# Optimization experiments

Measured on AMD Instinct MI355X. Metric: run time of the kernel, lower is better.

Reference implementation:

```python
import jax, jax.numpy as jnp
import numpy as np

N, E, D, H, DH, M = 100000, 1600000, 128, 8, 16, 3  # nodes, edges, model_dim, heads, head_dim, views
NEG = -1e9


def setup_inputs() -> dict:
    key = jax.random.key(0)
    ks = jax.random.split(key, 12)
    x = jax.random.normal(ks[0], (N, D), jnp.float32)
    src = jax.random.randint(ks[1], (E,), 0, N)
    dst = jax.random.randint(ks[2], (E,), 0, N)
    pi = jax.random.uniform(ks[3], (N, H, M), jnp.float32)
    pi = pi / pi.sum(-1, keepdims=True)  # router mixture over views
    view_w = jax.random.uniform(ks[4], (E, M), jnp.float32)
    s = 1.0 / np.sqrt(D)
    Wq = jax.random.normal(ks[5], (D, D), jnp.float32) * s
    Wk = jax.random.normal(ks[6], (D, D), jnp.float32) * s
    Wv = jax.random.normal(ks[7], (D, D), jnp.float32) * s
    bq = jax.random.normal(ks[8], (D,), jnp.float32) * 0.02
    bk = jax.random.normal(ks[9], (D,), jnp.float32) * 0.02
    bv = jax.random.normal(ks[10], (D,), jnp.float32) * 0.02
    return {"x": x, "pi": pi, "view_w": view_w, "Wq": Wq, "bq": bq,
            "Wk": Wk, "bk": bk, "Wv": Wv, "bv": bv, "src": src, "dst": dst}


def reference(x, pi, view_w, Wq, bq, Wk, bk, Wv, bv, src, dst):
    n = x.shape[0]
    q = (x @ Wq + bq).reshape(n, H, DH)
    k = (x @ Wk + bk).reshape(n, H, DH)
    v = (x @ Wv + bv).reshape(n, H, DH)
    # per-edge mixture weight: sum over views of pi[dst] * view_w  -> [E, H]
    mix = jnp.einsum('ehm,em->eh', pi[dst], view_w)
    raw = jnp.einsum('ehd,ehd->eh', q[dst], k[src]) / jnp.sqrt(jnp.float32(DH))
    scores = raw + jnp.log(jnp.clip(mix, 1e-8))  # adjacency_mode == 'bias'
    valid = mix > 0
    masked = jnp.where(valid, scores, NEG)
    # scatter-softmax over incoming edges per (node, head)
    smax = jax.ops.segment_max(masked, dst, num_segments=n)
    expv = jnp.where(valid, jnp.exp(masked - smax[dst]), 0.0)
    ssum = jax.ops.segment_sum(expv, dst, num_segments=n)
    attn = expv / jnp.maximum(ssum[dst], 1e-8)  # [E, H]
    # weighted scatter-sum aggregation -> [N, H, DH]
    node_states = jax.ops.segment_sum(v[src] * attn[:, :, None], dst, num_segments=n)
    return node_states, attn
```

## Files before the change

### kernel.cpp

```cpp
#include <hip/hip_runtime.h>
#include <hip/hip_bf16.h>
#include <math.h>

#define SCAN_CHUNK 2048

typedef _Float16 half8 __attribute__((ext_vector_type(8)));
typedef _Float16 half16v __attribute__((ext_vector_type(16)));
typedef float floatx4 __attribute__((ext_vector_type(4)));


__global__ void hist_kernel(const int* __restrict__ dst, int* __restrict__ counts, int e) {
    int i = blockIdx.x * blockDim.x + threadIdx.x;
    if (i < e) atomicAdd(&counts[dst[i]], 1);
}

__global__ __launch_bounds__(256) void scan_block_sums(const int* __restrict__ counts,
                                                       int* __restrict__ bsum, int n) {
    __shared__ int sd[256];
    int t = threadIdx.x;
    int base = blockIdx.x * SCAN_CHUNK + t * 8;
    int s = 0;
#pragma unroll
    for (int j = 0; j < 8; ++j) {
        int idx = base + j;
        if (idx < n) s += counts[idx];
    }
    sd[t] = s;
    __syncthreads();
    for (int off = 128; off > 0; off >>= 1) {
        if (t < off) sd[t] += sd[t + off];
        __syncthreads();
    }
    if (t == 0) bsum[blockIdx.x] = sd[0];
}

__global__ void scan_wave(int* bsum, int nb) {
    int lane = threadIdx.x;
    int orig = (lane < nb) ? bsum[lane] : 0;
    int v = orig;
    for (int off = 1; off < 64; off <<= 1) {
        int t = __shfl_up(v, off, 64);
        if (lane >= off) v += t;
    }
    if (lane < nb) bsum[lane] = v - orig;
}

__global__ __launch_bounds__(256) void scan_write(const int* __restrict__ counts,
                                                  const int* __restrict__ bsum,
                                                  int* __restrict__ row_ptr,
                                                  int* __restrict__ cursor,
                                                  int n, int total) {
    __shared__ int sd[256];
    int t = threadIdx.x;
    int base = blockIdx.x * SCAN_CHUNK + t * 8;
    int v[8];
    int s = 0;
#pragma unroll
    for (int j = 0; j < 8; ++j) {
        int idx = base + j;
        v[j] = (idx < n) ? counts[idx] : 0;
        s += v[j];
    }
    sd[t] = s;
    __syncthreads();
    for (int off = 1; off < 256; off <<= 1) {
        int tmp = 0;
        if (t >= off) tmp = sd[t - off];
        __syncthreads();
        if (t >= off) sd[t] += tmp;
        __syncthreads();
    }
    int run = bsum[blockIdx.x] + sd[t] - s;
#pragma unroll
    for (int j = 0; j < 8; ++j) {
        int idx = base + j;
        if (idx < n) {
            row_ptr[idx] = run;
            cursor[idx] = run;
            run += v[j];
        }
    }
    if (blockIdx.x == 0 && t == 0) row_ptr[n] = total;
}

__global__ void fill_csr(const int* __restrict__ dst, int* cursor,
                         int* __restrict__ csr, int e) {
    int i = blockIdx.x * blockDim.x + threadIdx.x;
    if (i < e) {
        int p = atomicAdd(&cursor[dst[i]], 1);
        csr[p] = i;
    }
}


__global__ __launch_bounds__(256) void convert_x(const float* __restrict__ x,
                                                 _Float16* __restrict__ xh, int total8) {
    int i = blockIdx.x * blockDim.x + threadIdx.x;
    if (i < total8) {
        const float4* s = (const float4*)x + i * 2;
        float4 a = s[0], b = s[1];
        half8 h;
        h[0] = (_Float16)a.x; h[1] = (_Float16)a.y; h[2] = (_Float16)a.z; h[3] = (_Float16)a.w;
        h[4] = (_Float16)b.x; h[5] = (_Float16)b.y; h[6] = (_Float16)b.z; h[7] = (_Float16)b.w;
        *((half8*)xh + i) = h;
    }
}

__global__ __launch_bounds__(256) void prep_w(const float* __restrict__ Wq,
                                              const float* __restrict__ Wk,
                                              const float* __restrict__ Wv,
                                              _Float16* __restrict__ wt) {
    const float* W = (blockIdx.x == 0) ? Wq : (blockIdx.x == 1) ? Wk : Wv;
    _Float16* out = wt + (size_t)blockIdx.x * 16384;
    int t = threadIdx.x;
    for (int r = 0; r < 64; ++r) {
        int idx = r * 256 + t;
        int k = idx >> 7, nn = idx & 127;
        out[nn * 128 + k] = (_Float16)W[idx];
    }
}


#define LDP 136

__global__ __launch_bounds__(256) void qkv_mfma(
    const _Float16* __restrict__ xh, const _Float16* __restrict__ wt,
    const float* __restrict__ bq, const float* __restrict__ bk,
    const float* __restrict__ bv,
    _Float16* __restrict__ qh, _Float16* __restrict__ kh, _Float16* __restrict__ vh,
    int n) {
    __shared__ __align__(16) _Float16 xs[128 * LDP];
    __shared__ __align__(16) _Float16 ws[128 * LDP];

    int t = threadIdx.x;
    int tile0 = blockIdx.x * 128;
    int sel = blockIdx.y;
    const _Float16* wsel = wt + (size_t)sel * 16384;
    const float* bias = (sel == 0) ? bq : (sel == 1) ? bk : bv;
    _Float16* out = (sel == 0) ? qh : (sel == 1) ? kh : vh;

#pragma unroll
    for (int r = 0; r < 8; ++r) {
        int id = r * 256 + t;
        int row = id >> 4, c8 = id & 15;
        int grow = tile0 + row;
        half8 val = (half8)(_Float16)0;
        if (grow < n) val = *((const half8*)(xh + (size_t)grow * 128) + c8);
        *((half8*)(xs + row * LDP) + c8) = val;
        half8 wv = *((const half8*)(wsel + row * 128) + c8);
        *((half8*)(ws + row * LDP) + c8) = wv;
    }
    __syncthreads();

    int wave = t >> 6, lane = t & 63;
    int wm = (wave & 1) * 64, wn = (wave >> 1) * 64;
    int lrow = lane & 15, quad = lane >> 4;

    floatx4 acc[4][4];
#pragma unroll
    for (int i = 0; i < 4; ++i)
#pragma unroll
        for (int j = 0; j < 4; ++j) acc[i][j] = (floatx4)0.f;

#pragma unroll
    for (int kk = 0; kk < 4; ++kk) {
        int kbase = kk * 32 + quad * 8;
        half8 a[4], b[4];
#pragma unroll
        for (int i = 0; i < 4; ++i)
            a[i] = *(const half8*)(xs + (wm + i * 16 + lrow) * LDP + kbase);
#pragma unroll
        for (int j = 0; j < 4; ++j)
            b[j] = *(const half8*)(ws + (wn + j * 16 + lrow) * LDP + kbase);
#pragma unroll
        for (int i = 0; i < 4; ++i)
#pragma unroll
            for (int j = 0; j < 4; ++j)
                acc[i][j] = __builtin_amdgcn_mfma_f32_16x16x32_f16(a[i], b[j], acc[i][j], 0, 0, 0);
    }

#pragma unroll
    for (int i = 0; i < 4; ++i) {
#pragma unroll
        for (int j = 0; j < 4; ++j) {
            int col = wn + j * 16 + lrow;
            float bv_ = bias[col];
#pragma unroll
            for (int r = 0; r < 4; ++r) {
                int row = wm + i * 16 + quad * 4 + r;
                int grow = tile0 + row;
                if (grow < n) out[(size_t)grow * 128 + col] = (_Float16)(acc[i][j][r] + bv_);
            }
        }
    }
}


__global__ __launch_bounds__(256) void edge_attn(
    const _Float16* __restrict__ qh, const _Float16* __restrict__ kh,
    const _Float16* __restrict__ vh, const float* __restrict__ pi,
    const float* __restrict__ view_w, const int* __restrict__ src,
    const int* __restrict__ row_ptr, const int* __restrict__ csr,
    float* __restrict__ node_out, float* __restrict__ invb,
    _Float16* __restrict__ pbuf, int n) {
    int t = threadIdx.x;
    int node = blockIdx.x * 32 + (t >> 3);
    int h = t & 7;
    if (node >= n) return;

    half16v qv = *(const half16v*)(qh + (size_t)node * 128 + h * 16);
    float qf[16];
#pragma unroll
    for (int j = 0; j < 16; ++j) qf[j] = (float)qv[j];

    float p0 = pi[node * 24 + h * 3 + 0];
    float p1 = pi[node * 24 + h * 3 + 1];
    float p2 = pi[node * 24 + h * 3 + 2];
    int beg = row_ptr[node], end = row_ptr[node + 1];

    float l = 0.f;
    float acc[16];
#pragma unroll
    for (int j = 0; j < 16; ++j) acc[j] = 0.f;

    int e_n = 0, s_n = 0;
    float wa_n = 0.f, wb_n = 0.f, wc_n = 0.f;
    if (beg < end) {
        e_n = csr[beg]; s_n = src[e_n];
        const float* vp_ = view_w + (size_t)e_n * 3;
        wa_n = vp_[0]; wb_n = vp_[1]; wc_n = vp_[2];
    }

    for (int i = beg; i < end; ++i) {
        int e = e_n, s0 = s_n;
        float wa = wa_n, wb = wb_n, wc = wc_n;

        const half16v* kp = (const half16v*)(kh + (size_t)s0 * 128 + h * 16);
        half16v kv = kp[0];
        const half16v* vp = (const half16v*)(vh + (size_t)s0 * 128 + h * 16);
        half16v vv = vp[0];

        if (i + 1 < end) {
            e_n = csr[i + 1]; s_n = src[e_n];
            const float* vpn = view_w + (size_t)e_n * 3;
            wa_n = vpn[0]; wb_n = vpn[1]; wc_n = vpn[2];
        }

        float mix = fmaf(p0, wa, fmaf(p1, wb, p2 * wc));
        float d = 0.f;
#pragma unroll
        for (int j = 0; j < 16; ++j) d = fmaf(qf[j], (float)kv[j], d);

        float p = (mix > 0.f) ? mix * __expf(d * 0.25f) : 0.f;
        pbuf[(size_t)e * 8 + h] = (_Float16)p;
        l += p;
#pragma unroll
        for (int j = 0; j < 16; ++j) acc[j] = fmaf(p, (float)vv[j], acc[j]);
    }

    float inv = 1.f / fmaxf(l, 1e-8f);
    invb[(size_t)node * 8 + h] = inv;

    float4* op = (float4*)(node_out + (size_t)node * 128 + h * 16);
#pragma unroll
    for (int j = 0; j < 4; ++j)
        op[j] = make_float4(acc[4 * j] * inv, acc[4 * j + 1] * inv,
                            acc[4 * j + 2] * inv, acc[4 * j + 3] * inv);
}


__global__ __launch_bounds__(256) void attn_norm(
    const _Float16* __restrict__ pbuf, const int* __restrict__ dst,
    const float* __restrict__ invb, float* __restrict__ attn_out, int e) {
    int i = blockIdx.x * blockDim.x + threadIdx.x;
    if (i < e) {
        int d = dst[i];
        half8 p = *((const half8*)pbuf + i);
        const float4* iv = (const float4*)(invb + (size_t)d * 8);
        float4 i0 = iv[0], i1 = iv[1];
        float4* op = (float4*)(attn_out + (size_t)i * 8);
        op[0] = make_float4((float)p[0] * i0.x, (float)p[1] * i0.y,
                            (float)p[2] * i0.z, (float)p[3] * i0.w);
        op[1] = make_float4((float)p[4] * i1.x, (float)p[5] * i1.y,
                            (float)p[6] * i1.z, (float)p[7] * i1.w);
    }
}


extern "C" void kernel_launch(void* const* d_in, const int* in_sizes, int n_in,
                              void* d_out, int out_size, void* d_ws, size_t ws_size,
                              hipStream_t stream) {
    const float* x  = (const float*)d_in[0];
    const float* pi = (const float*)d_in[1];
    const float* vw = (const float*)d_in[2];
    const float* Wq = (const float*)d_in[3];
    const float* bq = (const float*)d_in[4];
    const float* Wk = (const float*)d_in[5];
    const float* bk = (const float*)d_in[6];
    const float* Wv = (const float*)d_in[7];
    const float* bv = (const float*)d_in[8];
    const int* src  = (const int*)d_in[9];
    const int* dst  = (const int*)d_in[10];

    int n = in_sizes[0] / 128;
    int e = in_sizes[9];

    _Float16* xh = (_Float16*)d_ws;
    _Float16* qh = xh + (size_t)n * 128;
    _Float16* kh = qh + (size_t)n * 128;
    _Float16* vh = kh + (size_t)n * 128;
    _Float16* wt = vh + (size_t)n * 128;
    _Float16* pbuf = wt + 3 * 16384;
    float* invb  = (float*)(pbuf + (size_t)e * 8);
    int* counts  = (int*)(invb + (size_t)n * 8);
    int* cursor  = counts + n;
    int* row_ptr = cursor + n;
    int* csr     = row_ptr + n + 1;
    int* bsum    = csr + e;

    float* node_out = (float*)d_out;
    float* attn_out = node_out + (size_t)n * 128;

    hipMemsetAsync(counts, 0, (size_t)n * sizeof(int), stream);

    int eb = (e + 255) / 256;
    hist_kernel<<<eb, 256, 0, stream>>>(dst, counts, e);

    int nb = (n + SCAN_CHUNK - 1) / SCAN_CHUNK;
    scan_block_sums<<<nb, 256, 0, stream>>>(counts, bsum, n);
    scan_wave<<<1, 64, 0, stream>>>(bsum, nb);
    scan_write<<<nb, 256, 0, stream>>>(counts, bsum, row_ptr, cursor, n, e);
    fill_csr<<<eb, 256, 0, stream>>>(dst, cursor, csr, e);

    int tot8 = (n * 128) / 8;
    convert_x<<<(tot8 + 255) / 256, 256, 0, stream>>>(x, xh, tot8);
    prep_w<<<3, 256, 0, stream>>>(Wq, Wk, Wv, wt);

    int gtiles = (n + 127) / 128;
    qkv_mfma<<<dim3(gtiles, 3), 256, 0, stream>>>(xh, wt, bq, bk, bv, qh, kh, vh, n);

    int gb = (n + 31) / 32;
    edge_attn<<<gb, 256, 0, stream>>>(qh, kh, vh, pi, vw, src, row_ptr, csr,
                                      node_out, invb, pbuf, n);
    attn_norm<<<eb, 256, 0, stream>>>(pbuf, dst, invb, attn_out, e);
}
```

Measured before the change: 669.7 us.

## Sort nodes by in-degree for balanced edge attention and deepen K/V prefetch

Adds a degree histogram, a scan and a scatter that build a permutation of nodes ordered by in-degree. edge_attn then processes nodes in descending-degree order, so nodes in the same wavefront have similar loop trip counts and less divergence. The edge loop also prefetches K/V rows one edge ahead and indices two edges ahead, and uses the fdot2 builtin for the q·k dot product. The cost is three extra small kernels plus a memset, and a node order that scatters writes to node_out and invb rather than keeping them contiguous.

```diff
diff --git a/kernel.cpp b/kernel.cpp
--- a/kernel.cpp
+++ b/kernel.cpp
@@ -3,10 +3,18 @@
 #include <math.h>
 
 #define SCAN_CHUNK 2048
-
+#define DEG_BINS 256
+
+typedef _Float16 half2v __attribute__((ext_vector_type(2)));
 typedef _Float16 half8 __attribute__((ext_vector_type(8)));
 typedef _Float16 half16v __attribute__((ext_vector_type(16)));
 typedef float floatx4 __attribute__((ext_vector_type(4)));
+
+#if defined(__has_builtin)
+#if __has_builtin(__builtin_amdgcn_fdot2)
+#define USE_FDOT2 1
+#endif
+#endif
 
 
 __global__ void hist_kernel(const int* __restrict__ dst, int* __restrict__ counts, int e) {
@@ -89,6 +97,46 @@
     if (i < e) {
         int p = atomicAdd(&cursor[dst[i]], 1);
         csr[p] = i;
+    }
+}
+
+
+__global__ __launch_bounds__(256) void deg_hist(const int* __restrict__ counts,
+                                                int* __restrict__ bins, int n) {
+    int i = blockIdx.x * blockDim.x + threadIdx.x;
+    if (i < n) {
+        int d = counts[i];
+        if (d > DEG_BINS - 1) d = DEG_BINS - 1;
+        atomicAdd(&bins[d], 1);
+    }
+}
+
+__global__ __launch_bounds__(256) void deg_scan(const int* __restrict__ bins,
+                                                int* __restrict__ bcur) {
+    __shared__ int sd[256];
+    int t = threadIdx.x;
+    int v = bins[t];
+    sd[t] = v;
+    __syncthreads();
+    for (int off = 1; off < 256; off <<= 1) {
+        int tmp = 0;
+        if (t >= off) tmp = sd[t - off];
+        __syncthreads();
+        if (t >= off) sd[t] += tmp;
+        __syncthreads();
+    }
+    bcur[t] = sd[t] - v;
+}
+
+__global__ __launch_bounds__(256) void deg_scatter(const int* __restrict__ counts,
+                                                   int* __restrict__ bcur,
+                                                   int* __restrict__ perm, int n) {
+    int i = blockIdx.x * blockDim.x + threadIdx.x;
+    if (i < n) {
+        int d = counts[i];
+        if (d > DEG_BINS - 1) d = DEG_BINS - 1;
+        int p = atomicAdd(&bcur[d], 1);
+        perm[p] = i;
     }
 }
 
@@ -201,17 +249,18 @@
     const _Float16* __restrict__ vh, const float* __restrict__ pi,
     const float* __restrict__ view_w, const int* __restrict__ src,
     const int* __restrict__ row_ptr, const int* __restrict__ csr,
+    const int* __restrict__ perm,
     float* __restrict__ node_out, float* __restrict__ invb,
     _Float16* __restrict__ pbuf, int n) {
     int t = threadIdx.x;
-    int node = blockIdx.x * 32 + (t >> 3);
+    int gid = blockIdx.x * 32 + (t >> 3);
+    if (gid >= n) return;
+    int node = perm[n - 1 - gid];
     int h = t & 7;
-    if (node >= n) return;
-
-    half16v qv = *(const half16v*)(qh + (size_t)node * 128 + h * 16);
-    float qf[16];
-#pragma unroll
-    for (int j = 0; j < 16; ++j) qf[j] = (float)qv[j];
+
+    const half16v qv = *(const half16v*)(qh + (size_t)node * 128 + h * 16);
+    const _Float16* kbase = kh + h * 16;
+    const _Float16* vbase = vh + h * 16;
 
     float p0 = pi[node * 24 + h * 3 + 0];
     float p1 = pi[node * 24 + h * 3 + 1];
@@ -223,39 +272,62 @@
 #pragma unroll
     for (int j = 0; j < 16; ++j) acc[j] = 0.f;
 
-    int e_n = 0, s_n = 0;
-    float wa_n = 0.f, wb_n = 0.f, wc_n = 0.f;
+    int e0 = 0, s0 = 0, e1 = 0, s1 = 0;
+    float w0a = 0.f, w0b = 0.f, w0c = 0.f;
+    float w1a = 0.f, w1b = 0.f, w1c = 0.f;
+    half16v kc = (half16v)(_Float16)0, vc = (half16v)(_Float16)0;
+
     if (beg < end) {
-        e_n = csr[beg]; s_n = src[e_n];
-        const float* vp_ = view_w + (size_t)e_n * 3;
-        wa_n = vp_[0]; wb_n = vp_[1]; wc_n = vp_[2];
+        e0 = csr[beg]; s0 = src[e0];
+        const float* vp = view_w + (size_t)e0 * 3;
+        w0a = vp[0]; w0b = vp[1]; w0c = vp[2];
+        kc = *(const half16v*)(kbase + (size_t)s0 * 128);
+        vc = *(const half16v*)(vbase + (size_t)s0 * 128);
+    }
+    if (beg + 1 < end) {
+        e1 = csr[beg + 1]; s1 = src[e1];
+        const float* vp = view_w + (size_t)e1 * 3;
+        w1a = vp[0]; w1b = vp[1]; w1c = vp[2];
     }
 
     for (int i = beg; i < end; ++i) {
-        int e = e_n, s0 = s_n;
-        float wa = wa_n, wb = wb_n, wc = wc_n;
-
-        const half16v* kp = (const half16v*)(kh + (size_t)s0 * 128 + h * 16);
-        half16v kv = kp[0];
-        const half16v* vp = (const half16v*)(vh + (size_t)s0 * 128 + h * 16);
-        half16v vv = vp[0];
-
+        half16v kn = kc, vn = vc;
         if (i + 1 < end) {
-            e_n = csr[i + 1]; s_n = src[e_n];
-            const float* vpn = view_w + (size_t)e_n * 3;
-            wa_n = vpn[0]; wb_n = vpn[1]; wc_n = vpn[2];
+            kn = *(const half16v*)(kbase + (size_t)s1 * 128);
+            vn = *(const half16v*)(vbase + (size_t)s1 * 128);
         }
-
-        float mix = fmaf(p0, wa, fmaf(p1, wb, p2 * wc));
+        int e2 = 0, s2 = 0;
+        float w2a = 0.f, w2b = 0.f, w2c = 0.f;
+        if (i + 2 < end) {
+            e2 = csr[i + 2]; s2 = src[e2];
+            const float* vp = view_w + (size_t)e2 * 3;
+            w2a = vp[0]; w2b = vp[1]; w2c = vp[2];
+        }
+
+        float mix = fmaf(p0, w0a, fmaf(p1, w0b, p2 * w0c));
         float d = 0.f;
-#pragma unroll
-        for (int j = 0; j < 16; ++j) d = fmaf(qf[j], (float)kv[j], d);
+#ifdef USE_FDOT2
+#pragma unroll
+        for (int j = 0; j < 8; ++j) {
+            half2v a, b;
+            a[0] = qv[2 * j]; a[1] = qv[2 * j + 1];
+            b[0] = kc[2 * j]; b[1] = kc[2 * j + 1];
+            d = __builtin_amdgcn_fdot2(a, b, d, false);
+        }
+#else
+#pragma unroll
+        for (int j = 0; j < 16; ++j) d = fmaf((float)qv[j], (float)kc[j], d);
+#endif
 
         float p = (mix > 0.f) ? mix * __expf(d * 0.25f) : 0.f;
-        pbuf[(size_t)e * 8 + h] = (_Float16)p;
+        pbuf[(size_t)e0 * 8 + h] = (_Float16)p;
         l += p;
 #pragma unroll
-        for (int j = 0; j < 16; ++j) acc[j] = fmaf(p, (float)vv[j], acc[j]);
+        for (int j = 0; j < 16; ++j) acc[j] = fmaf(p, (float)vc[j], acc[j]);
+
+        e0 = e1; s0 = s1; w0a = w1a; w0b = w1b; w0c = w1c;
+        e1 = e2; s1 = s2; w1a = w2a; w1b = w2b; w1c = w2c;
+        kc = kn; vc = vn;
     }
 
     float inv = 1.f / fmaxf(l, 1e-8f);
@@ -317,14 +389,23 @@
     int* row_ptr = cursor + n;
     int* csr     = row_ptr + n + 1;
     int* bsum    = csr + e;
+    int* perm    = bsum + 64;
+    int* bins    = perm + n;
+    int* bcur    = bins + DEG_BINS;
 
     float* node_out = (float*)d_out;
     float* attn_out = node_out + (size_t)n * 128;
 
     hipMemsetAsync(counts, 0, (size_t)n * sizeof(int), stream);
+    hipMemsetAsync(bins, 0, DEG_BINS * sizeof(int), stream);
 
     int eb = (e + 255) / 256;
     hist_kernel<<<eb, 256, 0, stream>>>(dst, counts, e);
+
+    int nblk = (n + 255) / 256;
+    deg_hist<<<nblk, 256, 0, stream>>>(counts, bins, n);
+    deg_scan<<<1, 256, 0, stream>>>(bins, bcur);
+    deg_scatter<<<nblk, 256, 0, stream>>>(counts, bcur, perm, n);
 
     int nb = (n + SCAN_CHUNK - 1) / SCAN_CHUNK;
     scan_block_sums<<<nb, 256, 0, stream>>>(counts, bsum, n);
@@ -340,7 +421,7 @@
     qkv_mfma<<<dim3(gtiles, 3), 256, 0, stream>>>(xh, wt, bq, bk, bv, qh, kh, vh, n);
 
     int gb = (n + 31) / 32;
-    edge_attn<<<gb, 256, 0, stream>>>(qh, kh, vh, pi, vw, src, row_ptr, csr,
+    edge_attn<<<gb, 256, 0, stream>>>(qh, kh, vh, pi, vw, src, row_ptr, csr, perm,
                                       node_out, invb, pbuf, n);
     attn_norm<<<eb, 256, 0, stream>>>(pbuf, dst, invb, attn_out, e);
 }
```

Result: slower. 1.229 ms (+83.6%).

## Pack edge id with source in CSR and deepen edge-loop prefetch pipeline

Applied to the files above, without the earlier changes.

The CSR fill now stores an (edge id, src) pair, so the attention kernel no longer makes a dependent src lookup. The pair array lives in the attn output buffer, which is overwritten later. The edge loop is unrolled by two, with K/V/view_w prefetched two edges ahead and CSR entries four ahead, to hide gather latency. The q·k dot product uses packed fp16 fdot2 when available, which changes accumulation precision slightly. The extra in-flight registers may reduce occupancy.

```diff
diff --git a/kernel.cpp b/kernel.cpp
--- a/kernel.cpp
+++ b/kernel.cpp
@@ -4,9 +4,16 @@
 
 #define SCAN_CHUNK 2048
 
+typedef _Float16 half2v __attribute__((ext_vector_type(2)));
 typedef _Float16 half8 __attribute__((ext_vector_type(8)));
 typedef _Float16 half16v __attribute__((ext_vector_type(16)));
 typedef float floatx4 __attribute__((ext_vector_type(4)));
+
+#if defined(__has_builtin)
+#if __has_builtin(__builtin_amdgcn_fdot2)
+#define USE_FDOT2 1
+#endif
+#endif
 
 
 __global__ void hist_kernel(const int* __restrict__ dst, int* __restrict__ counts, int e) {
@@ -83,12 +90,12 @@
     if (blockIdx.x == 0 && t == 0) row_ptr[n] = total;
 }
 
-__global__ void fill_csr(const int* __restrict__ dst, int* cursor,
-                         int* __restrict__ csr, int e) {
+__global__ void fill_csr(const int* __restrict__ dst, const int* __restrict__ src,
+                         int* cursor, int2* __restrict__ csr2, int e) {
     int i = blockIdx.x * blockDim.x + threadIdx.x;
     if (i < e) {
         int p = atomicAdd(&cursor[dst[i]], 1);
-        csr[p] = i;
+        csr2[p] = make_int2(i, src[i]);
     }
 }
 
@@ -196,22 +203,78 @@
 }
 
 
+#define PREFETCH(S, idx)                                                      \
+    {                                                                         \
+        k##S = (half16v)(_Float16)0; v##S = (half16v)(_Float16)0;             \
+        w##S##0 = 0.f; w##S##1 = 0.f; w##S##2 = 0.f;                          \
+        if ((idx) < end) {                                                    \
+            k##S = *(const half16v*)(kbase + (size_t)m##S.y * 128);           \
+            v##S = *(const half16v*)(vbase + (size_t)m##S.y * 128);           \
+            const float* vp_ = view_w + (size_t)m##S.x * 3;                   \
+            w##S##0 = vp_[0]; w##S##1 = vp_[1]; w##S##2 = vp_[2];             \
+        }                                                                     \
+    }
+
+#ifdef USE_FDOT2
+#define DOT16(dres, kS)                                                       \
+    {                                                                         \
+        _Pragma("unroll")                                                     \
+        for (int j_ = 0; j_ < 8; ++j_) {                                      \
+            half2v a_, b_;                                                    \
+            a_[0] = qv[2 * j_]; a_[1] = qv[2 * j_ + 1];                       \
+            b_[0] = kS[2 * j_]; b_[1] = kS[2 * j_ + 1];                       \
+            dres = __builtin_amdgcn_fdot2(a_, b_, dres, false);               \
+        }                                                                     \
+    }
+#else
+#define DOT16(dres, kS)                                                       \
+    {                                                                         \
+        _Pragma("unroll")                                                     \
+        for (int j_ = 0; j_ < 16; ++j_)                                       \
+            dres = fmaf((float)qv[j_], (float)kS[j_], dres);                  \
+    }
+#endif
+
+#define COMPUTE(S, eidx, valid)                                               \
+    {                                                                         \
+        float mix_ = fmaf(p0, w##S##0, fmaf(p1, w##S##1, p2 * w##S##2));      \
+        float d_ = 0.f;                                                       \
+        DOT16(d_, k##S);                                                      \
+        float p_ = (mix_ > 0.f) ? mix_ * __expf(d_ * 0.25f) : 0.f;            \
+        if (valid) pbuf[(size_t)(eidx)*8 + h] = (_Float16)p_;                 \
+        l += p_;                                                              \
+        _Pragma("unroll")                                                     \
+        for (int j_ = 0; j_ < 16; ++j_)                                       \
+            acc[j_] = fmaf(p_, (float)v##S[j_], acc[j_]);                     \
+    }
+
+#define BODY(S0, S1, S2, S3, jj)                                              \
+    {                                                                         \
+        PREFETCH(S2, (jj) + 2);                                               \
+        PREFETCH(S3, (jj) + 3);                                               \
+        int eA_ = m##S0.x, eB_ = m##S1.x;                                     \
+        m##S0 = make_int2(0, 0); m##S1 = make_int2(0, 0);                     \
+        if ((jj) + 4 < end) m##S0 = csr2[(jj) + 4];                           \
+        if ((jj) + 5 < end) m##S1 = csr2[(jj) + 5];                           \
+        COMPUTE(S0, eA_, true);                                               \
+        COMPUTE(S1, eB_, (jj) + 1 < end);                                     \
+    }
+
 __global__ __launch_bounds__(256) void edge_attn(
     const _Float16* __restrict__ qh, const _Float16* __restrict__ kh,
     const _Float16* __restrict__ vh, const float* __restrict__ pi,
-    const float* __restrict__ view_w, const int* __restrict__ src,
-    const int* __restrict__ row_ptr, const int* __restrict__ csr,
+    const float* __restrict__ view_w,
+    const int* __restrict__ row_ptr, const int2* __restrict__ csr2,
     float* __restrict__ node_out, float* __restrict__ invb,
     _Float16* __restrict__ pbuf, int n) {
     int t = threadIdx.x;
     int node = blockIdx.x * 32 + (t >> 3);
+    if (node >= n) return;
     int h = t & 7;
-    if (node >= n) return;
-
-    half16v qv = *(const half16v*)(qh + (size_t)node * 128 + h * 16);
-    float qf[16];
-#pragma unroll
-    for (int j = 0; j < 16; ++j) qf[j] = (float)qv[j];
+
+    const half16v qv = *(const half16v*)(qh + (size_t)node * 128 + h * 16);
+    const _Float16* kbase = kh + h * 16;
+    const _Float16* vbase = vh + h * 16;
 
     float p0 = pi[node * 24 + h * 3 + 0];
     float p1 = pi[node * 24 + h * 3 + 1];
@@ -223,39 +286,26 @@
 #pragma unroll
     for (int j = 0; j < 16; ++j) acc[j] = 0.f;
 
-    int e_n = 0, s_n = 0;
-    float wa_n = 0.f, wb_n = 0.f, wc_n = 0.f;
-    if (beg < end) {
-        e_n = csr[beg]; s_n = src[e_n];
-        const float* vp_ = view_w + (size_t)e_n * 3;
-        wa_n = vp_[0]; wb_n = vp_[1]; wc_n = vp_[2];
-    }
-
-    for (int i = beg; i < end; ++i) {
-        int e = e_n, s0 = s_n;
-        float wa = wa_n, wb = wb_n, wc = wc_n;
-
-        const half16v* kp = (const half16v*)(kh + (size_t)s0 * 128 + h * 16);
-        half16v kv = kp[0];
-        const half16v* vp = (const half16v*)(vh + (size_t)s0 * 128 + h * 16);
-        half16v vv = vp[0];
-
-        if (i + 1 < end) {
-            e_n = csr[i + 1]; s_n = src[e_n];
-            const float* vpn = view_w + (size_t)e_n * 3;
-            wa_n = vpn[0]; wb_n = vpn[1]; wc_n = vpn[2];
-        }
-
-        float mix = fmaf(p0, wa, fmaf(p1, wb, p2 * wc));
-        float d = 0.f;
-#pragma unroll
-        for (int j = 0; j < 16; ++j) d = fmaf(qf[j], (float)kv[j], d);
-
-        float p = (mix > 0.f) ? mix * __expf(d * 0.25f) : 0.f;
-        pbuf[(size_t)e * 8 + h] = (_Float16)p;
-        l += p;
-#pragma unroll
-        for (int j = 0; j < 16; ++j) acc[j] = fmaf(p, (float)vv[j], acc[j]);
+    int2 mA = make_int2(0, 0), mB = make_int2(0, 0);
+    int2 mC = make_int2(0, 0), mD = make_int2(0, 0);
+    float wA0 = 0.f, wA1 = 0.f, wA2 = 0.f, wB0 = 0.f, wB1 = 0.f, wB2 = 0.f;
+    float wC0 = 0.f, wC1 = 0.f, wC2 = 0.f, wD0 = 0.f, wD1 = 0.f, wD2 = 0.f;
+    half16v kA = (half16v)(_Float16)0, vA = kA, kB = kA, vB = kA;
+    half16v kC = kA, vC = kA, kD = kA, vD = kA;
+
+    if (beg < end)     mA = csr2[beg];
+    if (beg + 1 < end) mB = csr2[beg + 1];
+    if (beg + 2 < end) mC = csr2[beg + 2];
+    if (beg + 3 < end) mD = csr2[beg + 3];
+    PREFETCH(A, beg);
+    PREFETCH(B, beg + 1);
+
+    for (int j = beg; j < end;) {
+        BODY(A, B, C, D, j);
+        j += 2;
+        if (j >= end) break;
+        BODY(C, D, A, B, j);
+        j += 2;
     }
 
     float inv = 1.f / fmaxf(l, 1e-8f);
@@ -315,11 +365,11 @@
     int* counts  = (int*)(invb + (size_t)n * 8);
     int* cursor  = counts + n;
     int* row_ptr = cursor + n;
-    int* csr     = row_ptr + n + 1;
-    int* bsum    = csr + e;
+    int* bsum    = row_ptr + n + 1;
 
     float* node_out = (float*)d_out;
     float* attn_out = node_out + (size_t)n * 128;
+    int2* csr2 = (int2*)attn_out;
 
     hipMemsetAsync(counts, 0, (size_t)n * sizeof(int), stream);
 
@@ -330,7 +380,7 @@
     scan_block_sums<<<nb, 256, 0, stream>>>(counts, bsum, n);
     scan_wave<<<1, 64, 0, stream>>>(bsum, nb);
     scan_write<<<nb, 256, 0, stream>>>(counts, bsum, row_ptr, cursor, n, e);
-    fill_csr<<<eb, 256, 0, stream>>>(dst, cursor, csr, e);
+    fill_csr<<<eb, 256, 0, stream>>>(dst, src, cursor, csr2, e);
 
     int tot8 = (n * 128) / 8;
     convert_x<<<(tot8 + 255) / 256, 256, 0, stream>>>(x, xh, tot8);
@@ -340,7 +390,7 @@
     qkv_mfma<<<dim3(gtiles, 3), 256, 0, stream>>>(xh, wt, bq, bk, bv, qh, kh, vh, n);
 
     int gb = (n + 31) / 32;
-    edge_attn<<<gb, 256, 0, stream>>>(qh, kh, vh, pi, vw, src, row_ptr, csr,
+    edge_attn<<<gb, 256, 0, stream>>>(qh, kh, vh, pi, vw, row_ptr, csr2,
                                       node_out, invb, pbuf, n);
     attn_norm<<<eb, 256, 0, stream>>>(pbuf, dst, invb, attn_out, e);
 }
```

Measured after the change: 646.3 us. 3.5% less time.

## Sort edge data into CSR order, precompute mixture weights, split heads across lanes

Applied to the files above, without the earlier changes.

fill_csr now writes the source index into CSR order and records each edge's CSR position. A new mix_kernel computes per-edge, per-head mixture weights into CSR order, reusing the attn output buffer as scratch. Edge reads in edge_attn then become contiguous instead of going through double indirection. edge_attn splits each head's 16-dim slice across two lanes (half8 loads, fdot2, one shuffle) with a deeper prefetch, and pbuf is stored in CSR order while attn_norm remaps through pos. The cost is an extra pass over the edges and an extra pos array.

```diff
diff --git a/kernel.cpp b/kernel.cpp
--- a/kernel.cpp
+++ b/kernel.cpp
@@ -4,9 +4,15 @@
 
 #define SCAN_CHUNK 2048
 
+typedef _Float16 half2v __attribute__((ext_vector_type(2)));
 typedef _Float16 half8 __attribute__((ext_vector_type(8)));
-typedef _Float16 half16v __attribute__((ext_vector_type(16)));
 typedef float floatx4 __attribute__((ext_vector_type(4)));
+
+#if defined(__has_builtin)
+#if __has_builtin(__builtin_amdgcn_fdot2)
+#define USE_FDOT2 1
+#endif
+#endif
 
 
 __global__ void hist_kernel(const int* __restrict__ dst, int* __restrict__ counts, int e) {
@@ -83,13 +89,41 @@
     if (blockIdx.x == 0 && t == 0) row_ptr[n] = total;
 }
 
-__global__ void fill_csr(const int* __restrict__ dst, int* cursor,
-                         int* __restrict__ csr, int e) {
+__global__ void fill_csr(const int* __restrict__ dst, const int* __restrict__ src,
+                         int* cursor, int* __restrict__ srcp,
+                         int* __restrict__ pos, int e) {
     int i = blockIdx.x * blockDim.x + threadIdx.x;
     if (i < e) {
         int p = atomicAdd(&cursor[dst[i]], 1);
-        csr[p] = i;
-    }
+        srcp[p] = src[i];
+        pos[i] = p;
+    }
+}
+
+
+__global__ __launch_bounds__(256) void mix_kernel(
+    const float* __restrict__ pi, const float* __restrict__ vw,
+    const int* __restrict__ dst, const int* __restrict__ pos,
+    float* __restrict__ mixf, int e) {
+    int i = blockIdx.x * blockDim.x + threadIdx.x;
+    if (i >= e) return;
+    int d = dst[i];
+    int p = pos[i];
+    float w0 = vw[3 * i], w1 = vw[3 * i + 1], w2 = vw[3 * i + 2];
+    const float4* pp = (const float4*)(pi + (size_t)d * 24);
+    float4 a0 = pp[0], a1 = pp[1], a2 = pp[2], a3 = pp[3], a4 = pp[4], a5 = pp[5];
+    float m[8];
+    m[0] = fmaf(a0.x, w0, fmaf(a0.y, w1, a0.z * w2));
+    m[1] = fmaf(a0.w, w0, fmaf(a1.x, w1, a1.y * w2));
+    m[2] = fmaf(a1.z, w0, fmaf(a1.w, w1, a2.x * w2));
+    m[3] = fmaf(a2.y, w0, fmaf(a2.z, w1, a2.w * w2));
+    m[4] = fmaf(a3.x, w0, fmaf(a3.y, w1, a3.z * w2));
+    m[5] = fmaf(a3.w, w0, fmaf(a4.x, w1, a4.y * w2));
+    m[6] = fmaf(a4.z, w0, fmaf(a4.w, w1, a5.x * w2));
+    m[7] = fmaf(a5.y, w0, fmaf(a5.z, w1, a5.w * w2));
+    float4* op = (float4*)(mixf + (size_t)p * 8);
+    op[0] = make_float4(m[0], m[1], m[2], m[3]);
+    op[1] = make_float4(m[4], m[5], m[6], m[7]);
 }
 
 
@@ -196,93 +230,111 @@
 }
 
 
-__global__ __launch_bounds__(256) void edge_attn(
+__global__ __launch_bounds__(64) void edge_attn(
     const _Float16* __restrict__ qh, const _Float16* __restrict__ kh,
-    const _Float16* __restrict__ vh, const float* __restrict__ pi,
-    const float* __restrict__ view_w, const int* __restrict__ src,
-    const int* __restrict__ row_ptr, const int* __restrict__ csr,
+    const _Float16* __restrict__ vh, const float* __restrict__ mixf,
+    const int* __restrict__ row_ptr, const int* __restrict__ srcp,
     float* __restrict__ node_out, float* __restrict__ invb,
     _Float16* __restrict__ pbuf, int n) {
     int t = threadIdx.x;
-    int node = blockIdx.x * 32 + (t >> 3);
-    int h = t & 7;
+    int node = blockIdx.x * 4 + (t >> 4);
     if (node >= n) return;
-
-    half16v qv = *(const half16v*)(qh + (size_t)node * 128 + h * 16);
-    float qf[16];
-#pragma unroll
-    for (int j = 0; j < 16; ++j) qf[j] = (float)qv[j];
-
-    float p0 = pi[node * 24 + h * 3 + 0];
-    float p1 = pi[node * 24 + h * 3 + 1];
-    float p2 = pi[node * 24 + h * 3 + 2];
+    int q16 = t & 15;
+    int h = q16 >> 1, sub = q16 & 1;
+    int off = h * 16 + sub * 8;
+
+    const half8 qv = *(const half8*)(qh + (size_t)node * 128 + off);
+    const _Float16* kbase = kh + off;
+    const _Float16* vbase = vh + off;
+
     int beg = row_ptr[node], end = row_ptr[node + 1];
 
     float l = 0.f;
-    float acc[16];
-#pragma unroll
-    for (int j = 0; j < 16; ++j) acc[j] = 0.f;
-
-    int e_n = 0, s_n = 0;
-    float wa_n = 0.f, wb_n = 0.f, wc_n = 0.f;
+    float a0 = 0.f, a1 = 0.f, a2 = 0.f, a3 = 0.f;
+    float a4 = 0.f, a5 = 0.f, a6 = 0.f, a7 = 0.f;
+
+    half8 kC = (half8)(_Float16)0, vC = (half8)(_Float16)0;
+    float mC = 0.f;
+    int sN = 0;
+    float mN = 0.f;
+
     if (beg < end) {
-        e_n = csr[beg]; s_n = src[e_n];
-        const float* vp_ = view_w + (size_t)e_n * 3;
-        wa_n = vp_[0]; wb_n = vp_[1]; wc_n = vp_[2];
-    }
-
-    for (int i = beg; i < end; ++i) {
-        int e = e_n, s0 = s_n;
-        float wa = wa_n, wb = wb_n, wc = wc_n;
-
-        const half16v* kp = (const half16v*)(kh + (size_t)s0 * 128 + h * 16);
-        half16v kv = kp[0];
-        const half16v* vp = (const half16v*)(vh + (size_t)s0 * 128 + h * 16);
-        half16v vv = vp[0];
-
-        if (i + 1 < end) {
-            e_n = csr[i + 1]; s_n = src[e_n];
-            const float* vpn = view_w + (size_t)e_n * 3;
-            wa_n = vpn[0]; wb_n = vpn[1]; wc_n = vpn[2];
+        int s0 = srcp[beg];
+        mC = mixf[(size_t)beg * 8 + h];
+        kC = *(const half8*)(kbase + (size_t)s0 * 128);
+        vC = *(const half8*)(vbase + (size_t)s0 * 128);
+    }
+    if (beg + 1 < end) {
+        sN = srcp[beg + 1];
+        mN = mixf[(size_t)(beg + 1) * 8 + h];
+    }
+
+    for (int j = beg; j < end; ++j) {
+        half8 kc = kC, vc = vC;
+        float mx = mC;
+        if (j + 1 < end) {
+            kC = *(const half8*)(kbase + (size_t)sN * 128);
+            vC = *(const half8*)(vbase + (size_t)sN * 128);
         }
-
-        float mix = fmaf(p0, wa, fmaf(p1, wb, p2 * wc));
+        mC = mN;
+        if (j + 2 < end) {
+            sN = srcp[j + 2];
+            mN = mixf[(size_t)(j + 2) * 8 + h];
+        }
+
         float d = 0.f;
-#pragma unroll
-        for (int j = 0; j < 16; ++j) d = fmaf(qf[j], (float)kv[j], d);
-
-        float p = (mix > 0.f) ? mix * __expf(d * 0.25f) : 0.f;
-        pbuf[(size_t)e * 8 + h] = (_Float16)p;
+#ifdef USE_FDOT2
+#pragma unroll
+        for (int jj = 0; jj < 4; ++jj) {
+            half2v x_, y_;
+            x_[0] = qv[2 * jj]; x_[1] = qv[2 * jj + 1];
+            y_[0] = kc[2 * jj]; y_[1] = kc[2 * jj + 1];
+            d = __builtin_amdgcn_fdot2(x_, y_, d, false);
+        }
+#else
+#pragma unroll
+        for (int jj = 0; jj < 8; ++jj) d = fmaf((float)qv[jj], (float)kc[jj], d);
+#endif
+        d += __shfl_xor(d, 1, 64);
+
+        float p = (mx > 0.f) ? mx * __expf(d * 0.25f) : 0.f;
+        if (sub == 0) pbuf[(size_t)j * 8 + h] = (_Float16)p;
         l += p;
-#pragma unroll
-        for (int j = 0; j < 16; ++j) acc[j] = fmaf(p, (float)vv[j], acc[j]);
+        a0 = fmaf(p, (float)vc[0], a0);
+        a1 = fmaf(p, (float)vc[1], a1);
+        a2 = fmaf(p, (float)vc[2], a2);
+        a3 = fmaf(p, (float)vc[3], a3);
+        a4 = fmaf(p, (float)vc[4], a4);
+        a5 = fmaf(p, (float)vc[5], a5);
+        a6 = fmaf(p, (float)vc[6], a6);
+        a7 = fmaf(p, (float)vc[7], a7);
     }
 
     float inv = 1.f / fmaxf(l, 1e-8f);
-    invb[(size_t)node * 8 + h] = inv;
-
-    float4* op = (float4*)(node_out + (size_t)node * 128 + h * 16);
-#pragma unroll
-    for (int j = 0; j < 4; ++j)
-        op[j] = make_float4(acc[4 * j] * inv, acc[4 * j + 1] * inv,
-                            acc[4 * j + 2] * inv, acc[4 * j + 3] * inv);
+    if (sub == 0) invb[(size_t)node * 8 + h] = inv;
+
+    float4* op = (float4*)(node_out + (size_t)node * 128 + off);
+    op[0] = make_float4(a0 * inv, a1 * inv, a2 * inv, a3 * inv);
+    op[1] = make_float4(a4 * inv, a5 * inv, a6 * inv, a7 * inv);
 }
 
 
 __global__ __launch_bounds__(256) void attn_norm(
     const _Float16* __restrict__ pbuf, const int* __restrict__ dst,
-    const float* __restrict__ invb, float* __restrict__ attn_out, int e) {
+    const int* __restrict__ pos, const float* __restrict__ invb,
+    float* __restrict__ attn_out, int e) {
     int i = blockIdx.x * blockDim.x + threadIdx.x;
     if (i < e) {
         int d = dst[i];
-        half8 p = *((const half8*)pbuf + i);
+        int p = pos[i];
+        half8 pv = *((const half8*)pbuf + p);
         const float4* iv = (const float4*)(invb + (size_t)d * 8);
         float4 i0 = iv[0], i1 = iv[1];
         float4* op = (float4*)(attn_out + (size_t)i * 8);
-        op[0] = make_float4((float)p[0] * i0.x, (float)p[1] * i0.y,
-                            (float)p[2] * i0.z, (float)p[3] * i0.w);
-        op[1] = make_float4((float)p[4] * i1.x, (float)p[5] * i1.y,
-                            (float)p[6] * i1.z, (float)p[7] * i1.w);
+        op[0] = make_float4((float)pv[0] * i0.x, (float)pv[1] * i0.y,
+                            (float)pv[2] * i0.z, (float)pv[3] * i0.w);
+        op[1] = make_float4((float)pv[4] * i1.x, (float)pv[5] * i1.y,
+                            (float)pv[6] * i1.z, (float)pv[7] * i1.w);
     }
 }
 
@@ -315,11 +367,13 @@
     int* counts  = (int*)(invb + (size_t)n * 8);
     int* cursor  = counts + n;
     int* row_ptr = cursor + n;
-    int* csr     = row_ptr + n + 1;
-    int* bsum    = csr + e;
+    int* bsum    = row_ptr + n + 1;
+    int* srcp    = bsum + 64;
+    int* pos     = srcp + e;
 
     float* node_out = (float*)d_out;
     float* attn_out = node_out + (size_t)n * 128;
+    float* mixf = attn_out;
 
     hipMemsetAsync(counts, 0, (size_t)n * sizeof(int), stream);
 
@@ -330,7 +384,8 @@
     scan_block_sums<<<nb, 256, 0, stream>>>(counts, bsum, n);
     scan_wave<<<1, 64, 0, stream>>>(bsum, nb);
     scan_write<<<nb, 256, 0, stream>>>(counts, bsum, row_ptr, cursor, n, e);
-    fill_csr<<<eb, 256, 0, stream>>>(dst, cursor, csr, e);
+    fill_csr<<<eb, 256, 0, stream>>>(dst, src, cursor, srcp, pos, e);
+    mix_kernel<<<eb, 256, 0, stream>>>(pi, vw, dst, pos, mixf, e);
 
     int tot8 = (n * 128) / 8;
     convert_x<<<(tot8 + 255) / 256, 256, 0, stream>>>(x, xh, tot8);
@@ -339,8 +394,8 @@
     int gtiles = (n + 127) / 128;
     qkv_mfma<<<dim3(gtiles, 3), 256, 0, stream>>>(xh, wt, bq, bk, bv, qh, kh, vh, n);
 
-    int gb = (n + 31) / 32;
-    edge_attn<<<gb, 256, 0, stream>>>(qh, kh, vh, pi, vw, src, row_ptr, csr,
-                                      node_out, invb, pbuf, n);
-    attn_norm<<<eb, 256, 0, stream>>>(pbuf, dst, invb, attn_out, e);
-}
+    int gb = (n + 3) / 4;
+    edge_attn<<<gb, 64, 0, stream>>>(qh, kh, vh, mixf, row_ptr, srcp,
+                                     node_out, invb, pbuf, n);
+    attn_norm<<<eb, 256, 0, stream>>>(pbuf, dst, pos, invb, attn_out, e);
+}
```

Measured after the change: 718.6 us. 7.3% more time.
